# Kernel optimization log

Hardware: AMD Instinct MI355X
Metric: run time of the kernel (lower is better)

The kernel has to match this reference:

```python
import jax, jax.numpy as jnp
import numpy as np

B, H, S, D = 4, 16, 2048, 64
TEMPERATURE = 8.0  # sqrt(D)
NEG = -1000000000.0

def setup_inputs() -> dict:
    key = jax.random.key(0)
    kq, kk, kv, km = jax.random.split(key, 4)
    q = jax.random.normal(kq, (B, H, S, D), dtype=jnp.float32)
    k = jax.random.normal(kk, (B, H, S, D), dtype=jnp.float32)
    v = jax.random.normal(kv, (B, H, S, D), dtype=jnp.float32)
    mask = jax.random.randint(km, (B, 1, S, S), 0, 2, dtype=jnp.int32)
    return {"q": q, "k": k, "v": v, "mask": mask}

def reference(q, k, v, mask):
    # scores: [B,H,S,S]
    scores = jnp.einsum('bhqd,bhkd->bhqk', q / TEMPERATURE, k)
    scores = jnp.where(mask == 1, NEG, scores)
    attn = jax.nn.softmax(scores, axis=-1)  # dropout p=0.0 -> identity
    out = jnp.einsum('bhqk,bhkd->bhqd', attn, v)
    return out
```

## Files before the change

### kernel.cpp

```cpp
#include <hip/hip_runtime.h>

#define NB 4
#define NH 16
#define SS 2048
#define DD 64
#define QT 256
#define KT 64
#define NT (SS / KT)
#define QSCALE 0.18033688011112042f
#define MASK_BITS_BYTES ((size_t)NB * SS * (SS / 8))

typedef __bf16 bf16x8 __attribute__((ext_vector_type(8)));
typedef __bf16 bf16x2 __attribute__((ext_vector_type(2)));
typedef float  floatx16 __attribute__((ext_vector_type(16)));
typedef unsigned long long u64t;

static_assert(sizeof(bf16x8) == 16, "bf16x8 must be 16B");

__device__ __forceinline__ int pack2(float a, float b) {
    bf16x2 v; v[0] = (__bf16)a; v[1] = (__bf16)b;
    return __builtin_bit_cast(int, v);
}

__global__ __launch_bounds__(256)
void pack_mask_kernel(const int* __restrict__ M, u64t* __restrict__ bits)
{
    const int w    = (blockIdx.x * 256 + threadIdx.x) >> 6;
    const int lane = threadIdx.x & 63;
    #pragma unroll 4
    for (int i = 0; i < 32; ++i) {
        const int gw   = i * 8192 + w;
        const size_t row = (size_t)(gw >> 5);
        const int word = gw & 31;
        const int mval = M[row * SS + (size_t)word * 64 + lane];
        const u64t b = __ballot(mval == 1);
        if (lane == 0) bits[gw] = b;
    }
}

template<bool USE_BITS>
__global__ __launch_bounds__(512, 4)
void attn_kernel(const float* __restrict__ Q, const float* __restrict__ K,
                 const float* __restrict__ V, const int* __restrict__ M,
                 const unsigned* __restrict__ MB, float* __restrict__ O)
{
    __shared__ __bf16 ks [2][KT][DD];
    __shared__ __bf16 vsT[2][DD][KT];

    const int t    = threadIdx.x;
    const int wave = t >> 6;
    const int lane = t & 63;
    const int l31  = lane & 31;
    const int h8   = lane >> 5;

    const int bh    = blockIdx.x & 63;
    const int qtile = blockIdx.x >> 6;
    const int b     = bh >> 4;
    const int q0    = qtile * QT + wave * 32;

    const size_t base = (size_t)bh * SS * DD;
    const float* Qb = Q + base;
    const float* Kb = K + base;
    const float* Vb = V + base;

    bf16x8 aq[4];
    {
        const float* qp = Qb + (size_t)(q0 + l31) * DD + 8 * h8;
        #pragma unroll
        for (int s = 0; s < 4; ++s) {
            float4 f0 = *(const float4*)(qp + 16 * s);
            float4 f1 = *(const float4*)(qp + 16 * s + 4);
            bf16x8 a;
            a[0] = (__bf16)(f0.x * QSCALE); a[1] = (__bf16)(f0.y * QSCALE);
            a[2] = (__bf16)(f0.z * QSCALE); a[3] = (__bf16)(f0.w * QSCALE);
            a[4] = (__bf16)(f1.x * QSCALE); a[5] = (__bf16)(f1.y * QSCALE);
            a[6] = (__bf16)(f1.z * QSCALE); a[7] = (__bf16)(f1.w * QSCALE);
            aq[s] = a;
        }
    }

    const int skey = t >> 3;
    const int sdc  = (t & 7) * 8;
    const int vk   = 2 * (t & 31);
    const int vdc  = (t >> 5) * 4;
    const int vcol = 16 * (vk >> 4) + 8 * ((vk >> 2) & 1) + (vk & 3) + 4 * ((vk >> 3) & 1);

    const float* kp0 = Kb + (size_t)skey * DD + sdc;
    const float* vp0 = Vb + (size_t)vk * DD + vdc;

    float4 ka0 = ((const float4*)kp0)[0];
    float4 ka1 = ((const float4*)kp0)[1];
    float4 va0 = *(const float4*)(vp0);
    float4 va1 = *(const float4*)(vp0 + DD);

    const u64t* mbrow = (const u64t*)MB + ((size_t)b * SS + q0 + l31) * (SS / 64);
    const int*  mrow  = M + (size_t)b * SS * SS + (size_t)(q0 + l31) * SS + 4 * h8;

    floatx16 o0, o1;
    #pragma unroll
    for (int i = 0; i < 16; ++i) { o0[i] = 0.f; o1[i] = 0.f; }
    float ls = 0.f;

    for (int tt = 0; tt < NT; ++tt) {
        const int cur = tt & 1;
        char* kb = (char*)&ks[cur][0][0];
        char* vb = (char*)&vsT[cur][0][0];

        {
            bf16x8 kw;
            kw[0]=(__bf16)ka0.x; kw[1]=(__bf16)ka0.y; kw[2]=(__bf16)ka0.z; kw[3]=(__bf16)ka0.w;
            kw[4]=(__bf16)ka1.x; kw[5]=(__bf16)ka1.y; kw[6]=(__bf16)ka1.z; kw[7]=(__bf16)ka1.w;
            *(bf16x8*)(kb + skey * 128 + ((16 * (t & 7)) ^ ((skey & 7) << 4))) = kw;
            #pragma unroll
            for (int i = 0; i < 4; ++i) {
                bf16x2 pr;
                pr[0] = (__bf16)(&va0.x)[i]; pr[1] = (__bf16)(&va1.x)[i];
                const int dim = vdc + i;
                *(bf16x2*)(vb + dim * 128 + ((2 * vcol) ^ ((dim & 7) << 4))) = pr;
            }
        }
        __syncthreads();

        u64t mall = 0;
        int4 mi[8];
        if (USE_BITS) {
            mall = mbrow[tt];
        } else {
            #pragma unroll
            for (int g = 0; g < 8; ++g)
                mi[g] = *(const int4*)(mrow + tt * KT + 8 * g);
        }

        {
            const int jn = ((tt + 1) * KT) & (SS - 1);
            const float* kn = kp0 + (size_t)jn * DD;
            ka0 = ((const float4*)kn)[0];
            ka1 = ((const float4*)kn)[1];
            const float* vn = vp0 + (size_t)jn * DD;
            va0 = *(const float4*)(vn);
            va1 = *(const float4*)(vn + DD);
        }

        #pragma unroll
        for (int half = 0; half < 2; ++half) {
            floatx16 c;
            #pragma unroll
            for (int i = 0; i < 16; ++i) c[i] = 0.f;
            __builtin_amdgcn_s_setprio(1);
            #pragma unroll
            for (int s = 0; s < 4; ++s) {
                const int r = 32 * half + l31;
                bf16x8 a = *(const bf16x8*)(kb + r * 128 +
                              ((32 * s + 16 * h8) ^ ((r & 7) << 4)));
                c = __builtin_amdgcn_mfma_f32_32x32x16_bf16(a, aq[s], c, 0, 0, 0);
            }
            __builtin_amdgcn_s_setprio(0);

            const unsigned mw = USE_BITS ? (unsigned)(mall >> (32 * half)) : 0u;
            const unsigned u  = mw >> (4 * h8);
            int pk[8];
            float psum = 0.f;
            #pragma unroll
            for (int g = 0; g < 8; ++g) {
                const int ia = 2 * g, ib = 2 * g + 1;
                float pa = __builtin_amdgcn_exp2f(c[ia]);
                float pb = __builtin_amdgcn_exp2f(c[ib]);
                bool ma, mb_;
                if (USE_BITS) {
                    ma  = (u >> ((ia & 3) + 8 * (ia >> 2))) & 1;
                    mb_ = (u >> ((ib & 3) + 8 * (ib >> 2))) & 1;
                } else {
                    const int g2 = 4 * half + (ia >> 2);
                    ma  = ((&mi[g2].x)[ia & 3] == 1);
                    mb_ = ((&mi[g2].x)[ib & 3] == 1);
                }
                pa = ma  ? 0.f : pa;
                pb = mb_ ? 0.f : pb;
                psum += pa + pb;
                pk[g] = pack2(pa, pb);
            }
            ls += psum;

            __builtin_amdgcn_s_setprio(1);
            #pragma unroll
            for (int s2 = 0; s2 < 2; ++s2) {
                int4 fw; fw.x = pk[4*s2]; fw.y = pk[4*s2+1]; fw.z = pk[4*s2+2]; fw.w = pk[4*s2+3];
                bf16x8 bp = __builtin_bit_cast(bf16x8, fw);
                const int c2 = 64 * half + 32 * s2 + 16 * h8;
                bf16x8 av0 = *(const bf16x8*)(vb + l31 * 128 +
                               (c2 ^ ((l31 & 7) << 4)));
                bf16x8 av1 = *(const bf16x8*)(vb + (32 + l31) * 128 +
                               (c2 ^ ((l31 & 7) << 4)));
                o0 = __builtin_amdgcn_mfma_f32_32x32x16_bf16(av0, bp, o0, 0, 0, 0);
                o1 = __builtin_amdgcn_mfma_f32_32x32x16_bf16(av1, bp, o1, 0, 0, 0);
            }
            __builtin_amdgcn_s_setprio(0);
        }
    }

    ls += __shfl_xor(ls, 32);
    float inv = 1.0f / ls;
    float* op = O + base + (size_t)(q0 + l31) * DD;
    #pragma unroll
    for (int s = 0; s < 4; ++s) {
        float4 st0, st1;
        st0.x = o0[4*s+0] * inv; st0.y = o0[4*s+1] * inv;
        st0.z = o0[4*s+2] * inv; st0.w = o0[4*s+3] * inv;
        st1.x = o1[4*s+0] * inv; st1.y = o1[4*s+1] * inv;
        st1.z = o1[4*s+2] * inv; st1.w = o1[4*s+3] * inv;
        *(float4*)(op + 8 * s + 4 * h8)      = st0;
        *(float4*)(op + 32 + 8 * s + 4 * h8) = st1;
    }
}

extern "C" void kernel_launch(void* const* d_in, const int* in_sizes, int n_in,
                              void* d_out, int out_size, void* d_ws, size_t ws_size,
                              hipStream_t stream) {
    (void)in_sizes; (void)n_in; (void)out_size;
    const float* q = (const float*)d_in[0];
    const float* k = (const float*)d_in[1];
    const float* v = (const float*)d_in[2];
    const int*   m = (const int*)d_in[3];
    float* out = (float*)d_out;
    dim3 grid(NB * NH * (SS / QT));

    if (ws_size >= MASK_BITS_BYTES) {
        u64t* bits = (u64t*)d_ws;
        pack_mask_kernel<<<dim3(2048), 256, 0, stream>>>(m, bits);
        attn_kernel<true><<<grid, 512, 0, stream>>>(q, k, v, m, (const unsigned*)bits, out);
    } else {
        attn_kernel<false><<<grid, 512, 0, stream>>>(q, k, v, m, (const unsigned*)nullptr, out);
    }
}
```

Before: 261.1 us.

## Pre-convert K and V to bf16 in a fused prepass and pad LDS rows

A new pre_kernel folds mask bit-packing together with a one-time conversion of K to bf16 and V to a transposed, permuted bf16 layout in workspace. The attention kernel then streams half as many bytes per K/V tile and copies them straight into shared memory with no per-block conversion. LDS tiles switch from XOR swizzling to a padded row stride of 72 to avoid bank conflicts. The cost is an extra prepass that reads and writes all of K and V, plus a workspace requirement of 34 MB; smaller workspaces fall back to the old paths.

```diff
diff --git a/kernel.cpp b/kernel.cpp
--- a/kernel.cpp
+++ b/kernel.cpp
@@ -7,8 +7,13 @@
 #define QT 256
 #define KT 64
 #define NT (SS / KT)
+#define KSP 72
 #define QSCALE 0.18033688011112042f
-#define MASK_BITS_BYTES ((size_t)NB * SS * (SS / 8))
+
+#define WS_BITS_BYTES ((size_t)NB * SS * (SS / 8))
+#define WS_KB_OFF  ((size_t)2  << 20)
+#define WS_VB_OFF  ((size_t)18 << 20)
+#define WS_FULL    ((size_t)34 << 20)
 
 typedef __bf16 bf16x8 __attribute__((ext_vector_type(8)));
 typedef __bf16 bf16x2 __attribute__((ext_vector_type(2)));
@@ -20,6 +25,13 @@
 __device__ __forceinline__ int pack2(float a, float b) {
     bf16x2 v; v[0] = (__bf16)a; v[1] = (__bf16)b;
     return __builtin_bit_cast(int, v);
+}
+
+__device__ __forceinline__ int vperm_col(int k) {
+    return 16 * (k >> 4) + 8 * ((k >> 2) & 1) + (k & 3) + 4 * ((k >> 3) & 1);
+}
+__device__ __forceinline__ int vperm_inv(int c) {
+    return 16 * ((c >> 4) & 3) + 8 * ((c >> 2) & 1) + 4 * ((c >> 3) & 1) + (c & 3);
 }
 
 __global__ __launch_bounds__(256)
@@ -38,14 +50,80 @@
     }
 }
 
-template<bool USE_BITS>
+__global__ __launch_bounds__(256)
+void pre_kernel(const float* __restrict__ K, const float* __restrict__ V,
+                const int* __restrict__ M, u64t* __restrict__ bits,
+                __bf16* __restrict__ KB, __bf16* __restrict__ VB)
+{
+    __shared__ float vt[64][68];
+    const int t = threadIdx.x;
+
+    if (blockIdx.x < 2048) {
+        const int bh = blockIdx.x >> 5;
+        const int tt = blockIdx.x & 31;
+        const size_t tb = (size_t)bh * SS * DD + (size_t)tt * (KT * DD);
+
+        {
+            const float* src = K + tb + t * 16;
+            __bf16* dst = KB + tb + t * 16;
+            float4 f0 = ((const float4*)src)[0];
+            float4 f1 = ((const float4*)src)[1];
+            float4 f2 = ((const float4*)src)[2];
+            float4 f3 = ((const float4*)src)[3];
+            bf16x8 o0, o1;
+            o0[0]=(__bf16)f0.x; o0[1]=(__bf16)f0.y; o0[2]=(__bf16)f0.z; o0[3]=(__bf16)f0.w;
+            o0[4]=(__bf16)f1.x; o0[5]=(__bf16)f1.y; o0[6]=(__bf16)f1.z; o0[7]=(__bf16)f1.w;
+            o1[0]=(__bf16)f2.x; o1[1]=(__bf16)f2.y; o1[2]=(__bf16)f2.z; o1[3]=(__bf16)f2.w;
+            o1[4]=(__bf16)f3.x; o1[5]=(__bf16)f3.y; o1[6]=(__bf16)f3.z; o1[7]=(__bf16)f3.w;
+            ((bf16x8*)dst)[0] = o0;
+            ((bf16x8*)dst)[1] = o1;
+        }
+
+        {
+            const int key = t >> 2, ds = (t & 3) * 16;
+            const float* src = V + tb + (size_t)key * DD + ds;
+            #pragma unroll
+            for (int i = 0; i < 4; ++i)
+                *(float4*)&vt[key][ds + 4 * i] = ((const float4*)src)[i];
+        }
+        __syncthreads();
+        {
+            const int dim = t >> 2, cb = (t & 3) * 16;
+            bf16x8 o0, o1;
+            #pragma unroll
+            for (int c = 0; c < 16; ++c) {
+                const float vvv = vt[vperm_inv(cb + c)][dim];
+                if (c < 8) o0[c] = (__bf16)vvv; else o1[c - 8] = (__bf16)vvv;
+            }
+            __bf16* dst = VB + tb + (size_t)dim * 64 + cb;
+            ((bf16x8*)dst)[0] = o0;
+            ((bf16x8*)dst)[1] = o1;
+        }
+    } else {
+        const int w    = ((blockIdx.x - 2048) * 256 + t) >> 6;
+        const int lane = t & 63;
+        #pragma unroll 4
+        for (int i = 0; i < 32; ++i) {
+            const int gw   = i * 8192 + w;
+            const size_t row = (size_t)(gw >> 5);
+            const int word = gw & 31;
+            const int mval = M[row * SS + (size_t)word * 64 + lane];
+            const u64t b = __ballot(mval == 1);
+            if (lane == 0) bits[gw] = b;
+        }
+    }
+}
+
+template<int MODE>
 __global__ __launch_bounds__(512, 4)
 void attn_kernel(const float* __restrict__ Q, const float* __restrict__ K,
                  const float* __restrict__ V, const int* __restrict__ M,
-                 const unsigned* __restrict__ MB, float* __restrict__ O)
+                 const unsigned* __restrict__ MB,
+                 const __bf16* __restrict__ KB, const __bf16* __restrict__ VB,
+                 float* __restrict__ O)
 {
-    __shared__ __bf16 ks [2][KT][DD];
-    __shared__ __bf16 vsT[2][DD][KT];
+    __shared__ __bf16 ks [2][KT][KSP];
+    __shared__ __bf16 vsT[2][DD][KSP];
 
     const int t    = threadIdx.x;
     const int wave = t >> 6;
@@ -59,13 +137,10 @@
     const int q0    = qtile * QT + wave * 32;
 
     const size_t base = (size_t)bh * SS * DD;
-    const float* Qb = Q + base;
-    const float* Kb = K + base;
-    const float* Vb = V + base;
 
     bf16x8 aq[4];
     {
-        const float* qp = Qb + (size_t)(q0 + l31) * DD + 8 * h8;
+        const float* qp = Q + base + (size_t)(q0 + l31) * DD + 8 * h8;
         #pragma unroll
         for (int s = 0; s < 4; ++s) {
             float4 f0 = *(const float4*)(qp + 16 * s);
@@ -79,19 +154,30 @@
         }
     }
 
+    const int srow = t >> 3;
+    const int sc8  = (t & 7) * 8;
+    const __bf16* kbp = KB + base + (size_t)srow * DD + sc8;
+    const __bf16* vbp = VB + base + (size_t)srow * DD + sc8;
+    bf16x8 kreg, vreg;
+
     const int skey = t >> 3;
     const int sdc  = (t & 7) * 8;
     const int vk   = 2 * (t & 31);
     const int vdc  = (t >> 5) * 4;
-    const int vcol = 16 * (vk >> 4) + 8 * ((vk >> 2) & 1) + (vk & 3) + 4 * ((vk >> 3) & 1);
-
-    const float* kp0 = Kb + (size_t)skey * DD + sdc;
-    const float* vp0 = Vb + (size_t)vk * DD + vdc;
-
-    float4 ka0 = ((const float4*)kp0)[0];
-    float4 ka1 = ((const float4*)kp0)[1];
-    float4 va0 = *(const float4*)(vp0);
-    float4 va1 = *(const float4*)(vp0 + DD);
+    const int vcol = vperm_col(vk);
+    const float* kp0 = K + base + (size_t)skey * DD + sdc;
+    const float* vp0 = V + base + (size_t)vk * DD + vdc;
+    float4 ka0, ka1, va0, va1;
+
+    if constexpr (MODE == 2) {
+        kreg = *(const bf16x8*)kbp;
+        vreg = *(const bf16x8*)vbp;
+    } else {
+        ka0 = ((const float4*)kp0)[0];
+        ka1 = ((const float4*)kp0)[1];
+        va0 = *(const float4*)(vp0);
+        va1 = *(const float4*)(vp0 + DD);
+    }
 
     const u64t* mbrow = (const u64t*)MB + ((size_t)b * SS + q0 + l31) * (SS / 64);
     const int*  mrow  = M + (size_t)b * SS * SS + (size_t)(q0 + l31) * SS + 4 * h8;
@@ -103,27 +189,27 @@
 
     for (int tt = 0; tt < NT; ++tt) {
         const int cur = tt & 1;
-        char* kb = (char*)&ks[cur][0][0];
-        char* vb = (char*)&vsT[cur][0][0];
-
-        {
+
+        if constexpr (MODE == 2) {
+            *(bf16x8*)&ks [cur][srow][sc8] = kreg;
+            *(bf16x8*)&vsT[cur][srow][sc8] = vreg;
+        } else {
             bf16x8 kw;
             kw[0]=(__bf16)ka0.x; kw[1]=(__bf16)ka0.y; kw[2]=(__bf16)ka0.z; kw[3]=(__bf16)ka0.w;
             kw[4]=(__bf16)ka1.x; kw[5]=(__bf16)ka1.y; kw[6]=(__bf16)ka1.z; kw[7]=(__bf16)ka1.w;
-            *(bf16x8*)(kb + skey * 128 + ((16 * (t & 7)) ^ ((skey & 7) << 4))) = kw;
+            *(bf16x8*)&ks[cur][skey][sdc] = kw;
             #pragma unroll
             for (int i = 0; i < 4; ++i) {
                 bf16x2 pr;
                 pr[0] = (__bf16)(&va0.x)[i]; pr[1] = (__bf16)(&va1.x)[i];
-                const int dim = vdc + i;
-                *(bf16x2*)(vb + dim * 128 + ((2 * vcol) ^ ((dim & 7) << 4))) = pr;
+                *(bf16x2*)&vsT[cur][vdc + i][vcol] = pr;
             }
         }
         __syncthreads();
 
         u64t mall = 0;
         int4 mi[8];
-        if (USE_BITS) {
+        if constexpr (MODE >= 1) {
             mall = mbrow[tt];
         } else {
             #pragma unroll
@@ -131,7 +217,11 @@
                 mi[g] = *(const int4*)(mrow + tt * KT + 8 * g);
         }
 
-        {
+        if constexpr (MODE == 2) {
+            const size_t jn = (size_t)((tt + 1) & (NT - 1)) * (KT * DD);
+            kreg = *(const bf16x8*)(kbp + jn);
+            vreg = *(const bf16x8*)(vbp + jn);
+        } else {
             const int jn = ((tt + 1) * KT) & (SS - 1);
             const float* kn = kp0 + (size_t)jn * DD;
             ka0 = ((const float4*)kn)[0];
@@ -149,14 +239,12 @@
             __builtin_amdgcn_s_setprio(1);
             #pragma unroll
             for (int s = 0; s < 4; ++s) {
-                const int r = 32 * half + l31;
-                bf16x8 a = *(const bf16x8*)(kb + r * 128 +
-                              ((32 * s + 16 * h8) ^ ((r & 7) << 4)));
+                bf16x8 a = *(const bf16x8*)&ks[cur][32 * half + l31][16 * s + 8 * h8];
                 c = __builtin_amdgcn_mfma_f32_32x32x16_bf16(a, aq[s], c, 0, 0, 0);
             }
             __builtin_amdgcn_s_setprio(0);
 
-            const unsigned mw = USE_BITS ? (unsigned)(mall >> (32 * half)) : 0u;
+            const unsigned mw = (MODE >= 1) ? (unsigned)(mall >> (32 * half)) : 0u;
             const unsigned u  = mw >> (4 * h8);
             int pk[8];
             float psum = 0.f;
@@ -166,7 +254,7 @@
                 float pa = __builtin_amdgcn_exp2f(c[ia]);
                 float pb = __builtin_amdgcn_exp2f(c[ib]);
                 bool ma, mb_;
-                if (USE_BITS) {
+                if constexpr (MODE >= 1) {
                     ma  = (u >> ((ia & 3) + 8 * (ia >> 2))) & 1;
                     mb_ = (u >> ((ib & 3) + 8 * (ib >> 2))) & 1;
                 } else {
@@ -186,11 +274,8 @@
             for (int s2 = 0; s2 < 2; ++s2) {
                 int4 fw; fw.x = pk[4*s2]; fw.y = pk[4*s2+1]; fw.z = pk[4*s2+2]; fw.w = pk[4*s2+3];
                 bf16x8 bp = __builtin_bit_cast(bf16x8, fw);
-                const int c2 = 64 * half + 32 * s2 + 16 * h8;
-                bf16x8 av0 = *(const bf16x8*)(vb + l31 * 128 +
-                               (c2 ^ ((l31 & 7) << 4)));
-                bf16x8 av1 = *(const bf16x8*)(vb + (32 + l31) * 128 +
-                               (c2 ^ ((l31 & 7) << 4)));
+                bf16x8 av0 = *(const bf16x8*)&vsT[cur][l31]     [32 * half + 16 * s2 + 8 * h8];
+                bf16x8 av1 = *(const bf16x8*)&vsT[cur][32 + l31][32 * half + 16 * s2 + 8 * h8];
                 o0 = __builtin_amdgcn_mfma_f32_32x32x16_bf16(av0, bp, o0, 0, 0, 0);
                 o1 = __builtin_amdgcn_mfma_f32_32x32x16_bf16(av1, bp, o1, 0, 0, 0);
             }
@@ -224,11 +309,20 @@
     float* out = (float*)d_out;
     dim3 grid(NB * NH * (SS / QT));
 
-    if (ws_size >= MASK_BITS_BYTES) {
+    if (ws_size >= WS_FULL) {
+        u64t*   bits = (u64t*)d_ws;
+        __bf16* kb16 = (__bf16*)((char*)d_ws + WS_KB_OFF);
+        __bf16* vb16 = (__bf16*)((char*)d_ws + WS_VB_OFF);
+        pre_kernel<<<dim3(4096), 256, 0, stream>>>(k, v, m, bits, kb16, vb16);
+        attn_kernel<2><<<grid, 512, 0, stream>>>(q, k, v, m, (const unsigned*)bits,
+                                                 kb16, vb16, out);
+    } else if (ws_size >= WS_BITS_BYTES) {
         u64t* bits = (u64t*)d_ws;
         pack_mask_kernel<<<dim3(2048), 256, 0, stream>>>(m, bits);
-        attn_kernel<true><<<grid, 512, 0, stream>>>(q, k, v, m, (const unsigned*)bits, out);
+        attn_kernel<1><<<grid, 512, 0, stream>>>(q, k, v, m, (const unsigned*)bits,
+                                                 nullptr, nullptr, out);
     } else {
-        attn_kernel<false><<<grid, 512, 0, stream>>>(q, k, v, m, (const unsigned*)nullptr, out);
-    }
-}
+        attn_kernel<0><<<grid, 512, 0, stream>>>(q, k, v, m, nullptr,
+                                                 nullptr, nullptr, out);
+    }
+}
```

Result: slower. 273.6 us (+4.8%).
